# Optimization experiments

Hardware: AMD Instinct MI355X
Metric: run time of the kernel (lower is better)

## Reference

```python
import jax, jax.numpy as jnp
import numpy as np

N_HEAD = 16
D_HEAD = 64
SCALE = 1.0 / D_HEAD ** 0.5


def setup_inputs() -> dict:
    key = jax.random.key(0)
    k1, k2, k3, k4 = jax.random.split(key, 4)
    bsz, qlen, d_embed, d_model = 4, 1024, 768, 1024
    return {
        "word_emb": jax.random.normal(k1, (bsz, qlen, d_embed), dtype=jnp.float32),
        "emb_w": jax.random.normal(k2, (d_embed, d_model), dtype=jnp.float32) * 0.02,
        "emb_b": jnp.zeros((d_model,), dtype=jnp.float32),
        "qkv_w0": jax.random.normal(k3, (d_model, 3 * N_HEAD * D_HEAD), dtype=jnp.float32) * 0.02,
        "qkv_w1": jax.random.normal(k4, (d_model, 3 * N_HEAD * D_HEAD), dtype=jnp.float32) * 0.02,
    }


def _mha(h, qkv_w):
    # h: [qlen, bsz, d_model]
    qlen, bsz, _ = h.shape
    heads = h @ qkv_w  # [qlen, bsz, 3*n_head*d_head]
    head_q, head_k, head_v = jnp.split(heads, 3, axis=-1)
    head_q = head_q.reshape(qlen, bsz, N_HEAD, D_HEAD)
    head_k = head_k.reshape(qlen, bsz, N_HEAD, D_HEAD)
    head_v = head_v.reshape(qlen, bsz, N_HEAD, D_HEAD)
    # explicit score materialization, faithful to the source einsum pattern
    attn_score = jnp.einsum('ibnd,jbnd->ijbn', head_q, head_k) * SCALE
    attn_prob = jax.nn.softmax(attn_score, axis=1)  # softmax over klen (dim=1)
    attn_vec = jnp.einsum('ijbn,jbnd->ibnd', attn_prob, head_v)
    attn_vec = attn_vec.reshape(qlen, bsz, N_HEAD * D_HEAD)
    return attn_vec, attn_prob


def reference(word_emb, emb_w, emb_b, qkv_w0, qkv_w1):
    # word_emb: [bsz, qlen, d_embed] -> [qlen, bsz, d_embed]
    h = jnp.transpose(word_emb, (1, 0, 2))
    h = h @ emb_w + emb_b  # emb_proj since d_embed != d_model
    # NOTE: the source computes pos_emb and word_emb + pos_emb, but then
    # overwrites with core_out = self.drop(word_emb), discarding pos_emb.
    # Dropout is identity in reference (eval) mode, so core_out == h.
    core_out = h
    core_out, attn_maps = _mha(core_out, qkv_w0)
    core_out, attn_maps = _mha(core_out, qkv_w1)
    return core_out, attn_maps
```

## Files before the change

kernel.cpp:

```cpp
#include <hip/hip_runtime.h>

#define LOG2E 1.44269504088896340736f

typedef __attribute__((ext_vector_type(8))) short short8;
typedef __attribute__((ext_vector_type(4))) short short4v;
typedef __attribute__((ext_vector_type(4))) float floatx4;

__device__ __forceinline__ float bf2f(short s) {
    union { float f; unsigned u; } v; v.u = ((unsigned)(unsigned short)s) << 16; return v.f;
}
__device__ __forceinline__ short f2bf(float f) {
    union { float f; unsigned u; } v; v.f = f;
    unsigned u = v.u;
    u += 0x7FFFu + ((u >> 16) & 1u);
    return (short)(u >> 16);
}

__device__ __forceinline__ void gl_lds16(const void* g, void* l) {
    __builtin_amdgcn_global_load_lds((const __attribute__((address_space(1))) void*)g,
                                     (__attribute__((address_space(3))) void*)l, 16, 0, 0);
}

__device__ __forceinline__ void wcast_tile(const float* __restrict__ W,
                                           short* __restrict__ Wt, int K, int N,
                                           int n0, int k0, int t) {
    __shared__ float tile[64][65];
    int r = t >> 2, c4 = (t & 3) * 16;
    const float* src = W + (size_t)(k0 + r) * N + n0 + c4;
    float4 f0 = *(const float4*)(src);
    float4 f1 = *(const float4*)(src + 4);
    float4 f2 = *(const float4*)(src + 8);
    float4 f3 = *(const float4*)(src + 12);
    tile[r][c4 + 0] = f0.x;  tile[r][c4 + 1] = f0.y;  tile[r][c4 + 2] = f0.z;  tile[r][c4 + 3] = f0.w;
    tile[r][c4 + 4] = f1.x;  tile[r][c4 + 5] = f1.y;  tile[r][c4 + 6] = f1.z;  tile[r][c4 + 7] = f1.w;
    tile[r][c4 + 8] = f2.x;  tile[r][c4 + 9] = f2.y;  tile[r][c4 + 10] = f2.z; tile[r][c4 + 11] = f2.w;
    tile[r][c4 + 12] = f3.x; tile[r][c4 + 13] = f3.y; tile[r][c4 + 14] = f3.z; tile[r][c4 + 15] = f3.w;
    __syncthreads();
    short* dst = Wt + (size_t)(n0 + r) * K + k0 + c4;
    short8 o1, o2;
#pragma unroll
    for (int q = 0; q < 8; ++q) o1[q] = f2bf(tile[c4 + q][r]);
#pragma unroll
    for (int q = 0; q < 8; ++q) o2[q] = f2bf(tile[c4 + 8 + q][r]);
    *(short8*)(dst) = o1;
    *(short8*)(dst + 8) = o2;
}

__global__ __launch_bounds__(256) void prep(const float* __restrict__ we,
                                            const float* __restrict__ emb_w,
                                            const float* __restrict__ qkv_w0,
                                            const float* __restrict__ qkv_w1,
                                            short* __restrict__ A0,
                                            short* __restrict__ WtE,
                                            short* __restrict__ Wt0,
                                            short* __restrict__ Wt1) {
    int bid = blockIdx.x, t = threadIdx.x;
    if (bid < 1536) {
        int e = bid * 256 + t;
        int m = e / 96, dc = (e % 96) * 8;
        int b = m & 3, s = m >> 2;
        const float* src = we + (size_t)(b * 1024 + s) * 768 + dc;
        float4 f0 = *(const float4*)(src);
        float4 f1 = *(const float4*)(src + 4);
        short8 o;
        o[0] = f2bf(f0.x); o[1] = f2bf(f0.y); o[2] = f2bf(f0.z); o[3] = f2bf(f0.w);
        o[4] = f2bf(f1.x); o[5] = f2bf(f1.y); o[6] = f2bf(f1.z); o[7] = f2bf(f1.w);
        *(short8*)(A0 + (size_t)m * 768 + dc) = o;
    } else if (bid < 1728) {
        int tt = bid - 1536;
        wcast_tile(emb_w, WtE, 768, 1024, (tt & 15) * 64, (tt >> 4) * 64, t);
    } else if (bid < 2496) {
        int tt = bid - 1728;
        wcast_tile(qkv_w0, Wt0, 1024, 3072, (tt % 48) * 64, (tt / 48) * 64, t);
    } else {
        int tt = bid - 2496;
        wcast_tile(qkv_w1, Wt1, 1024, 3072, (tt % 48) * 64, (tt / 48) * 64, t);
    }
}

template <int PACK>
__global__ __launch_bounds__(256) void gemm_bt(const short* __restrict__ A,
                                               const short* __restrict__ Bt,
                                               short* __restrict__ C,
                                               const float* __restrict__ bias,
                                               int K, int N,
                                               short* __restrict__ Qp,
                                               short* __restrict__ Kp,
                                               short* __restrict__ Vp) {
    __shared__ __align__(16) short sA[128 * 64];
    __shared__ __align__(16) short sB[128 * 64];
    int NT = N >> 7;
    int bid = blockIdx.x;
    int xcd = bid & 7, t8 = bid >> 3;
    int n0 = (t8 % NT) * 128;
    int m0 = (xcd * 4 + t8 / NT) * 128;
    int tid = threadIdx.x;
    int lane = tid & 63, w = tid >> 6;
    int wm = (w >> 1) * 64, wn = (w & 1) * 64;
    int l15 = lane & 15, quad = lane >> 4;
    int lrow = lane >> 3, lchunk = (lane & 7) ^ lrow;

    floatx4 zero = {0.f, 0.f, 0.f, 0.f};
    floatx4 acc[4][4];
#pragma unroll
    for (int i = 0; i < 4; ++i)
#pragma unroll
        for (int j = 0; j < 4; ++j) acc[i][j] = zero;

    for (int k0 = 0; k0 < K; k0 += 64) {
#pragma unroll
        for (int c = 0; c < 4; ++c) {
            int r0 = w * 32 + c * 8;
            int row = r0 + lrow;
            gl_lds16(A + (size_t)(m0 + row) * K + k0 + lchunk * 8, sA + r0 * 64);
            gl_lds16(Bt + (size_t)(n0 + row) * K + k0 + lchunk * 8, sB + r0 * 64);
        }
        __syncthreads();
#pragma unroll
        for (int h = 0; h < 2; ++h) {
            int sw = ((h * 4 + quad) ^ (l15 & 7)) * 8;
            short8 af[4], bfr[4];
#pragma unroll
            for (int i = 0; i < 4; ++i) {
                af[i]  = *(const short8*)(sA + (wm + i * 16 + l15) * 64 + sw);
                bfr[i] = *(const short8*)(sB + (wn + i * 16 + l15) * 64 + sw);
            }
#pragma unroll
            for (int i = 0; i < 4; ++i)
#pragma unroll
                for (int j = 0; j < 4; ++j)
                    acc[i][j] = __builtin_amdgcn_mfma_f32_16x16x32_bf16(bfr[j], af[i], acc[i][j], 0, 0, 0);
        }
        __syncthreads();
    }
#pragma unroll
    for (int i = 0; i < 4; ++i) {
        int row = m0 + wm + i * 16 + l15;
#pragma unroll
        for (int j = 0; j < 4; ++j) {
            int colb = n0 + wn + j * 16 + quad * 4;
            if (PACK == 0) {
                float4 bv = bias ? *(const float4*)(bias + colb) : float4{0.f, 0.f, 0.f, 0.f};
                short4v st;
                st[0] = f2bf(acc[i][j][0] + bv.x);
                st[1] = f2bf(acc[i][j][1] + bv.y);
                st[2] = f2bf(acc[i][j][2] + bv.z);
                st[3] = f2bf(acc[i][j][3] + bv.w);
                *(short4v*)(C + (size_t)row * N + colb) = st;
            } else {
                int sel = colb >> 10, nn = colb & 1023;
                int bn = ((row & 3) << 4) + (nn >> 6);
                size_t idx = (size_t)bn * 65536 + (size_t)(row >> 2) * 64 + (nn & 63);
                float sc = (sel == 0) ? 0.125f : 1.0f;
                short4v st;
#pragma unroll
                for (int r = 0; r < 4; ++r) st[r] = f2bf(acc[i][j][r] * sc);
                short* dst = (sel == 0) ? Qp : (sel == 1 ? Kp : Vp);
                *(short4v*)(dst + idx) = st;
            }
        }
    }
}

__global__ __launch_bounds__(256) void pack_v(const short* __restrict__ Vp,
                                              short* __restrict__ Vtp) {
    __shared__ short vt[64][72];
    int bn = blockIdx.y;
    int t0 = blockIdx.x * 64;
    int t = threadIdx.x;
#pragma unroll
    for (int h = 0; h < 2; ++h) {
        int c = t + h * 256;
        int tt = c >> 3, off = (c & 7) * 8;
        short8 v = *(const short8*)(Vp + (size_t)bn * 65536 + (size_t)(t0 + tt) * 64 + off);
#pragma unroll
        for (int e = 0; e < 8; ++e) vt[tt][off + e] = v[e];
    }
    __syncthreads();
#pragma unroll
    for (int h = 0; h < 2; ++h) {
        int c = t + h * 256;
        int d = c >> 3, joff = (c & 7) * 8;
        short8 o;
#pragma unroll
        for (int e = 0; e < 8; ++e) o[e] = vt[joff + e][d];
        *(short8*)(Vtp + (size_t)bn * 65536 + (size_t)d * 1024 + t0 + joff) = o;
    }
}

template <bool L2>
__global__ __launch_bounds__(256) void fattn(const short* __restrict__ Qp,
                                             const short* __restrict__ Kp,
                                             const short* __restrict__ Vtp,
                                             void* __restrict__ Optr,
                                             float* __restrict__ linv,
                                             short* __restrict__ Pp) {
    __shared__ __align__(16) short sK[2][32 * 64];
    __shared__ __align__(16) short sV[2][64 * 40];
    __shared__ __align__(16) short plds[4][2][32 * 32];
    int bid = blockIdx.x;
    int xcd = bid & 7, rr = bid >> 3;
    int bn = xcd * 8 + (rr & 7);
    int iblk = rr >> 3;
    int tid = threadIdx.x, w = tid >> 6, lane = tid & 63;
    int i0 = iblk * 128 + w * 32;
    int b = bn >> 4, n = bn & 15;
    int l15 = lane & 15, quad = lane >> 4;
    const short* Qb = Qp + (size_t)bn * 65536;
    const char* Kb = (const char*)(Kp + (size_t)bn * 65536);
    const char* Vb = (const char*)(Vtp + (size_t)bn * 65536);

    int kr_ = lane >> 3, ko_ = lane & 7;
    size_t koff = (size_t)kr_ * 128 + ((ko_ ^ kr_) * 16);
    int vr_[5], vc_[5];
#pragma unroll
    for (int c = 0; c < 5; ++c) {
        int beta = c * 1024 + lane * 16;
        vr_[c] = beta / 80;
        vc_[c] = (beta % 80) & 63;
    }

#define KCALL(B, J0, c) \
    gl_lds16(Kb + (size_t)((J0) + 8 * (c)) * 128 + koff, (char*)sK[B] + (c) * 1024)
#define VCALL(B, J0, c) \
    gl_lds16(Vb + (size_t)vr_[c] * 2048 + (size_t)(J0) * 2 + vc_[c], (char*)sV[B] + (c) * 1024)
#define STAGE(B, J0) do { \
        if (w == 0)      { KCALL(B, J0, 0); KCALL(B, J0, 1); } \
        else if (w == 1) { KCALL(B, J0, 2); KCALL(B, J0, 3); } \
        else if (w == 2) { VCALL(B, J0, 0); VCALL(B, J0, 1); VCALL(B, J0, 2); } \
        else             { VCALL(B, J0, 3); VCALL(B, J0, 4); } \
    } while (0)

    short8 qf[2][2];
#pragma unroll
    for (int ib = 0; ib < 2; ++ib) {
        qf[ib][0] = *(const short8*)(Qb + (i0 + ib * 16 + l15) * 64 + quad * 8);
        qf[ib][1] = *(const short8*)(Qb + (i0 + ib * 16 + l15) * 64 + 32 + quad * 8);
    }
    floatx4 zero = {0.f, 0.f, 0.f, 0.f};
    floatx4 o[2][4];
#pragma unroll
    for (int ib = 0; ib < 2; ++ib)
#pragma unroll
        for (int tt = 0; tt < 4; ++tt) o[ib][tt] = zero;
    float lsum[2] = {0.f, 0.f};

    size_t ptb = (size_t)bn * 1048576 + (size_t)(i0 >> 5) * 32768;

    STAGE(0, 0);
    __syncthreads();

    int buf = 0;
#pragma unroll 2
    for (int j0 = 0; j0 < 1024; j0 += 32) {
        if (j0 + 32 < 1024) STAGE(buf ^ 1, j0 + 32);
        short* pw = plds[w][buf];
        int r7 = l15 & 7;
#pragma unroll
        for (int jb = 0; jb < 2; ++jb) {
            const short* kbase = sK[buf] + (jb * 16 + l15) * 64;
            short8 kf0 = *(const short8*)(kbase + ((quad ^ r7) * 8));
            short8 kf1 = *(const short8*)(kbase + (((4 + quad) ^ r7) * 8));
#pragma unroll
            for (int ib = 0; ib < 2; ++ib) {
                floatx4 s = zero;
                s = __builtin_amdgcn_mfma_f32_16x16x32_bf16(kf0, qf[ib][0], s, 0, 0, 0);
                s = __builtin_amdgcn_mfma_f32_16x16x32_bf16(kf1, qf[ib][1], s, 0, 0, 0);
                short4v pk;
                float ls = 0.f;
#pragma unroll
                for (int r = 0; r < 4; ++r) {
                    float p = __builtin_amdgcn_exp2f(s[r] * LOG2E);
                    ls += p;
                    pk[r] = f2bf(p);
                }
                lsum[ib] += ls;
                *(short4v*)(pw + (ib * 16 + l15) * 32 + jb * 16 + quad * 4) = pk;
            }
        }
        short8 pa[2];
        pa[0] = *(const short8*)(pw + l15 * 32 + quad * 8);
        pa[1] = *(const short8*)(pw + (16 + l15) * 32 + quad * 8);
        if (L2) {
            short* pt = Pp + ptb + (j0 >> 5) * 1024;
            *(short8*)(pt + l15 * 32 + quad * 8) = pa[0];
            *(short8*)(pt + (16 + l15) * 32 + quad * 8) = pa[1];
        }
#pragma unroll
        for (int tt = 0; tt < 4; ++tt) {
            short8 vf = *(const short8*)(sV[buf] + (tt * 16 + l15) * 40 + quad * 8);
#pragma unroll
            for (int ib = 0; ib < 2; ++ib)
                o[ib][tt] = __builtin_amdgcn_mfma_f32_16x16x32_bf16(vf, pa[ib], o[ib][tt], 0, 0, 0);
        }
        __syncthreads();
        buf ^= 1;
    }
#undef STAGE
#undef KCALL
#undef VCALL

    float rinv[2];
#pragma unroll
    for (int ib = 0; ib < 2; ++ib) {
        float t = lsum[ib];
        t += __shfl_xor(t, 16);
        t += __shfl_xor(t, 32);
        rinv[ib] = 1.f / t;
    }
    if (L2 && quad == 0) {
        linv[bn * 1024 + i0 + l15] = rinv[0];
        linv[bn * 1024 + i0 + 16 + l15] = rinv[1];
    }
#pragma unroll
    for (int ib = 0; ib < 2; ++ib)
#pragma unroll
        for (int tt = 0; tt < 4; ++tt) {
            int row = i0 + ib * 16 + l15;
            int colb = n * 64 + tt * 16 + quad * 4;
            size_t idx = (size_t)(row * 4 + b) * 1024 + colb;
            if (L2) {
                float4 v;
                v.x = o[ib][tt][0] * rinv[ib];
                v.y = o[ib][tt][1] * rinv[ib];
                v.z = o[ib][tt][2] * rinv[ib];
                v.w = o[ib][tt][3] * rinv[ib];
                *(float4*)((float*)Optr + idx) = v;
            } else {
                short4v st;
#pragma unroll
                for (int r = 0; r < 4; ++r) st[r] = f2bf(o[ib][tt][r] * rinv[ib]);
                *(short4v*)((short*)Optr + idx) = st;
            }
        }
}

__global__ __launch_bounds__(256) void pfin(const short* __restrict__ Pp,
                                            const float* __restrict__ linv,
                                            float* __restrict__ Pout) {
    __shared__ short sP[64 * 512];
    int j0 = blockIdx.x * 32, i0 = blockIdx.y * 16;
    int t = threadIdx.x;
    size_t tbase = (size_t)(i0 >> 5) * 32768 + (size_t)(j0 >> 5) * 1024 + (i0 & 16) * 32;
#pragma unroll
    for (int h = 0; h < 16; ++h) {
        int c = t + h * 256;
        int bn = c >> 6, rem = c & 63, ii = rem >> 2, part = rem & 3;
        short8 v = *(const short8*)(Pp + (size_t)bn * 1048576 + tbase + ii * 32 + part * 8);
        float li = linv[bn * 1024 + i0 + ii];
        short8 sv;
#pragma unroll
        for (int e = 0; e < 8; ++e) sv[e] = f2bf(bf2f(v[e]) * li);
        *(short8*)(sP + bn * 512 + ii * 32 + part * 8) = sv;
    }
    __syncthreads();
    int ii = t >> 4, q = t & 15;
    float* dst = Pout + (size_t)(i0 + ii) * 65536 + j0 * 64 + q * 128;
#pragma unroll
    for (int e4 = 0; e4 < 32; ++e4) {
        int pos = q * 128 + e4 * 4;
        int jj = pos >> 6, bnb = pos & 63;
        float4 v;
        v.x = bf2f(sP[(bnb + 0) * 512 + ii * 32 + jj]);
        v.y = bf2f(sP[(bnb + 1) * 512 + ii * 32 + jj]);
        v.z = bf2f(sP[(bnb + 2) * 512 + ii * 32 + jj]);
        v.w = bf2f(sP[(bnb + 3) * 512 + ii * 32 + jj]);
        *(float4*)(dst + e4 * 4) = v;
    }
}

extern "C" void kernel_launch(void* const* d_in, const int* in_sizes, int n_in,
                              void* d_out, int out_size, void* d_ws, size_t ws_size,
                              hipStream_t stream) {
    const float* word_emb = (const float*)d_in[0];
    const float* emb_w    = (const float*)d_in[1];
    const float* emb_b    = (const float*)d_in[2];
    const float* qkv_w0   = (const float*)d_in[3];
    const float* qkv_w1   = (const float*)d_in[4];
    float* out0 = (float*)d_out;
    float* out1 = out0 + 4194304;

    char* ws = (char*)d_ws;
    short* A0    = (short*)(ws);
    short* WtE   = (short*)(ws + 6291456);
    short* Wt0   = (short*)(ws + 7864320);
    short* Wt1   = (short*)(ws + 14155776);
    short* hbuf  = (short*)(ws + 20447232);
    short* h2    = (short*)(ws + 28835840);
    short* Qp    = (short*)(ws + 37224448);
    short* Kp    = (short*)(ws + 45613056);
    short* Vp    = (short*)(ws + 54001664);
    short* Vtp   = (short*)(ws + 62390272);
    float* linv  = (float*)(ws + 70778880);
    short* Pp    = (short*)(ws + 71041024);

    prep<<<3264, 256, 0, stream>>>(word_emb, emb_w, qkv_w0, qkv_w1, A0, WtE, Wt0, Wt1);

    gemm_bt<0><<<256, 256, 0, stream>>>(A0, WtE, hbuf, emb_b, 768, 1024,
                                        nullptr, nullptr, nullptr);
    gemm_bt<1><<<768, 256, 0, stream>>>(hbuf, Wt0, nullptr, nullptr, 1024, 3072,
                                        Qp, Kp, Vp);
    pack_v<<<dim3(16, 64), 256, 0, stream>>>(Vp, Vtp);
    fattn<false><<<512, 256, 0, stream>>>(Qp, Kp, Vtp, (void*)h2, nullptr, nullptr);
    gemm_bt<1><<<768, 256, 0, stream>>>(h2, Wt1, nullptr, nullptr, 1024, 3072,
                                        Qp, Kp, Vp);
    pack_v<<<dim3(16, 64), 256, 0, stream>>>(Vp, Vtp);
    fattn<true><<<512, 256, 0, stream>>>(Qp, Kp, Vtp, (void*)out0, linv, Pp);
    pfin<<<dim3(32, 64), 256, 0, stream>>>(Pp, linv, out1);
}
```

Measured before the change: 630.6 us.

## Fuse V transpose into QKV GEMM epilogue and use nontemporal streaming stores

The QKV GEMM epilogue now writes V directly in transposed [bn][d][t] layout with scalar 2-byte stores, so the separate pack_v kernel and the intermediate Vp buffer are removed for both attention layers. The large attention-probability and output writes in fattn and pfin, and the Pp reads, switch to nontemporal load/store builtins to avoid polluting cache. The aim is fewer launches and less round-trip memory traffic. The scattered scalar stores for V are uncoalesced and could make the GEMM epilogue slower.

Result: slower. 1.224 ms (+94.1%).

```diff
diff --git a/kernel.cpp b/kernel.cpp
--- a/kernel.cpp
+++ b/kernel.cpp
@@ -86,7 +86,7 @@
                                                int K, int N,
                                                short* __restrict__ Qp,
                                                short* __restrict__ Kp,
-                                               short* __restrict__ Vp) {
+                                               short* __restrict__ Vtp) {
     __shared__ __align__(16) short sA[128 * 64];
     __shared__ __align__(16) short sB[128 * 64];
     int NT = N >> 7;
@@ -150,41 +150,23 @@
             } else {
                 int sel = colb >> 10, nn = colb & 1023;
                 int bn = ((row & 3) << 4) + (nn >> 6);
-                size_t idx = (size_t)bn * 65536 + (size_t)(row >> 2) * 64 + (nn & 63);
-                float sc = (sel == 0) ? 0.125f : 1.0f;
-                short4v st;
-#pragma unroll
-                for (int r = 0; r < 4; ++r) st[r] = f2bf(acc[i][j][r] * sc);
-                short* dst = (sel == 0) ? Qp : (sel == 1 ? Kp : Vp);
-                *(short4v*)(dst + idx) = st;
+                int t = row >> 2;
+                if (sel == 2) {
+                    int d = nn & 63;
+#pragma unroll
+                    for (int r = 0; r < 4; ++r)
+                        Vtp[(size_t)bn * 65536 + (size_t)(d + r) * 1024 + t] =
+                            f2bf(acc[i][j][r]);
+                } else {
+                    float sc = (sel == 0) ? 0.125f : 1.0f;
+                    short4v st;
+#pragma unroll
+                    for (int r = 0; r < 4; ++r) st[r] = f2bf(acc[i][j][r] * sc);
+                    short* dst = (sel == 0) ? Qp : Kp;
+                    *(short4v*)(dst + (size_t)bn * 65536 + (size_t)t * 64 + (nn & 63)) = st;
+                }
             }
         }
-    }
-}
-
-__global__ __launch_bounds__(256) void pack_v(const short* __restrict__ Vp,
-                                              short* __restrict__ Vtp) {
-    __shared__ short vt[64][72];
-    int bn = blockIdx.y;
-    int t0 = blockIdx.x * 64;
-    int t = threadIdx.x;
-#pragma unroll
-    for (int h = 0; h < 2; ++h) {
-        int c = t + h * 256;
-        int tt = c >> 3, off = (c & 7) * 8;
-        short8 v = *(const short8*)(Vp + (size_t)bn * 65536 + (size_t)(t0 + tt) * 64 + off);
-#pragma unroll
-        for (int e = 0; e < 8; ++e) vt[tt][off + e] = v[e];
-    }
-    __syncthreads();
-#pragma unroll
-    for (int h = 0; h < 2; ++h) {
-        int c = t + h * 256;
-        int d = c >> 3, joff = (c & 7) * 8;
-        short8 o;
-#pragma unroll
-        for (int e = 0; e < 8; ++e) o[e] = vt[joff + e][d];
-        *(short8*)(Vtp + (size_t)bn * 65536 + (size_t)d * 1024 + t0 + joff) = o;
     }
 }
 
@@ -283,8 +265,8 @@
         pa[1] = *(const short8*)(pw + (16 + l15) * 32 + quad * 8);
         if (L2) {
             short* pt = Pp + ptb + (j0 >> 5) * 1024;
-            *(short8*)(pt + l15 * 32 + quad * 8) = pa[0];
-            *(short8*)(pt + (16 + l15) * 32 + quad * 8) = pa[1];
+            __builtin_nontemporal_store(pa[0], (short8*)(pt + l15 * 32 + quad * 8));
+            __builtin_nontemporal_store(pa[1], (short8*)(pt + (16 + l15) * 32 + quad * 8));
         }
 #pragma unroll
         for (int tt = 0; tt < 4; ++tt) {
@@ -320,12 +302,12 @@
             int colb = n * 64 + tt * 16 + quad * 4;
             size_t idx = (size_t)(row * 4 + b) * 1024 + colb;
             if (L2) {
-                float4 v;
-                v.x = o[ib][tt][0] * rinv[ib];
-                v.y = o[ib][tt][1] * rinv[ib];
-                v.z = o[ib][tt][2] * rinv[ib];
-                v.w = o[ib][tt][3] * rinv[ib];
-                *(float4*)((float*)Optr + idx) = v;
+                floatx4 v;
+                v[0] = o[ib][tt][0] * rinv[ib];
+                v[1] = o[ib][tt][1] * rinv[ib];
+                v[2] = o[ib][tt][2] * rinv[ib];
+                v[3] = o[ib][tt][3] * rinv[ib];
+                __builtin_nontemporal_store(v, (floatx4*)((float*)Optr + idx));
             } else {
                 short4v st;
 #pragma unroll
@@ -346,7 +328,8 @@
     for (int h = 0; h < 16; ++h) {
         int c = t + h * 256;
         int bn = c >> 6, rem = c & 63, ii = rem >> 2, part = rem & 3;
-        short8 v = *(const short8*)(Pp + (size_t)bn * 1048576 + tbase + ii * 32 + part * 8);
+        short8 v = __builtin_nontemporal_load(
+            (const short8*)(Pp + (size_t)bn * 1048576 + tbase + ii * 32 + part * 8));
         float li = linv[bn * 1024 + i0 + ii];
         short8 sv;
 #pragma unroll
@@ -360,12 +343,12 @@
     for (int e4 = 0; e4 < 32; ++e4) {
         int pos = q * 128 + e4 * 4;
         int jj = pos >> 6, bnb = pos & 63;
-        float4 v;
-        v.x = bf2f(sP[(bnb + 0) * 512 + ii * 32 + jj]);
-        v.y = bf2f(sP[(bnb + 1) * 512 + ii * 32 + jj]);
-        v.z = bf2f(sP[(bnb + 2) * 512 + ii * 32 + jj]);
-        v.w = bf2f(sP[(bnb + 3) * 512 + ii * 32 + jj]);
-        *(float4*)(dst + e4 * 4) = v;
+        floatx4 v;
+        v[0] = bf2f(sP[(bnb + 0) * 512 + ii * 32 + jj]);
+        v[1] = bf2f(sP[(bnb + 1) * 512 + ii * 32 + jj]);
+        v[2] = bf2f(sP[(bnb + 2) * 512 + ii * 32 + jj]);
+        v[3] = bf2f(sP[(bnb + 3) * 512 + ii * 32 + jj]);
+        __builtin_nontemporal_store(v, (floatx4*)(dst + e4 * 4));
     }
 }
 
@@ -389,7 +372,6 @@
     short* h2    = (short*)(ws + 28835840);
     short* Qp    = (short*)(ws + 37224448);
     short* Kp    = (short*)(ws + 45613056);
-    short* Vp    = (short*)(ws + 54001664);
     short* Vtp   = (short*)(ws + 62390272);
     float* linv  = (float*)(ws + 70778880);
     short* Pp    = (short*)(ws + 71041024);
@@ -399,12 +381,10 @@
     gemm_bt<0><<<256, 256, 0, stream>>>(A0, WtE, hbuf, emb_b, 768, 1024,
                                         nullptr, nullptr, nullptr);
     gemm_bt<1><<<768, 256, 0, stream>>>(hbuf, Wt0, nullptr, nullptr, 1024, 3072,
-                                        Qp, Kp, Vp);
-    pack_v<<<dim3(16, 64), 256, 0, stream>>>(Vp, Vtp);
+                                        Qp, Kp, Vtp);
     fattn<false><<<512, 256, 0, stream>>>(Qp, Kp, Vtp, (void*)h2, nullptr, nullptr);
     gemm_bt<1><<<768, 256, 0, stream>>>(h2, Wt1, nullptr, nullptr, 1024, 3072,
-                                        Qp, Kp, Vp);
-    pack_v<<<dim3(16, 64), 256, 0, stream>>>(Vp, Vtp);
+                                        Qp, Kp, Vtp);
     fattn<true><<<512, 256, 0, stream>>>(Qp, Kp, Vtp, (void*)out0, linv, Pp);
     pfin<<<dim3(32, 64), 256, 0, stream>>>(Pp, linv, out1);
 }
```
